# Kernel optimization log

Hardware: AMD Instinct MI355X
Metric: run time of the kernel (lower is better)

## Reference

```python
import jax, jax.numpy as jnp
import numpy as np

N_NODES = 50000
N_EDGES = 800000
N_GRAPHS = 128
F_IN = 128
HID = 64
EDGE_DIM = 16
H1, H2 = 4, 2
NEG_SLOPE = 0.2


def _glorot(key, shape, fan_in):
    return jax.random.normal(key, shape, dtype=jnp.float32) / np.sqrt(fan_in)


def setup_inputs() -> dict:
    key = jax.random.key(0)
    ks = jax.random.split(key, 20)
    x = jax.random.normal(ks[0], (N_NODES, F_IN), dtype=jnp.float32)
    edge_attr = jax.random.normal(ks[1], (N_EDGES, EDGE_DIM), dtype=jnp.float32)
    edge_index = jax.random.randint(ks[2], (2, N_EDGES), 0, N_NODES, dtype=jnp.int32)
    # evenly spread graph ids so every graph is non-empty (sorted)
    batch = (jnp.arange(N_NODES, dtype=jnp.int32) * N_GRAPHS) // N_NODES
    p = {
        'W1': _glorot(ks[3], (F_IN, H1 * HID), F_IN),
        'a_src1': _glorot(ks[4], (H1, HID), HID),
        'a_dst1': _glorot(ks[5], (H1, HID), HID),
        'We1': _glorot(ks[6], (EDGE_DIM, H1 * HID), EDGE_DIM),
        'a_e1': _glorot(ks[7], (H1, HID), HID),
        'b1': jnp.zeros((H1 * HID,), jnp.float32),
        'W2': _glorot(ks[8], (H1 * HID, H2 * HID), H1 * HID),
        'a_src2': _glorot(ks[9], (H2, HID), HID),
        'a_dst2': _glorot(ks[10], (H2, HID), HID),
        'We2': _glorot(ks[11], (EDGE_DIM, H2 * HID), EDGE_DIM),
        'a_e2': _glorot(ks[12], (H2, HID), HID),
        'b2': jnp.zeros((HID,), jnp.float32),
        'Wr': _glorot(ks[13], (HID, 1), HID),
        'br': jnp.zeros((1,), jnp.float32),
    }
    return dict(x=x, edge_attr=edge_attr, edge_index=edge_index, batch=batch, **p)


def _segment_softmax(scores, seg, num_segments):
    # scores: [E, H], softmax grouped by seg (destination node)
    m = jax.ops.segment_max(scores, seg, num_segments)
    m = jnp.where(jnp.isfinite(m), m, 0.0)
    ex = jnp.exp(scores - m[seg])
    s = jax.ops.segment_sum(ex, seg, num_segments)
    return ex / (s[seg] + 1e-16)


def _add_self_loops(edge_index, edge_attr, n):
    # PyG add_self_loops with fill_value='mean': per-dst mean of edge_attr
    src, dst = edge_index[0], edge_index[1]
    cnt = jax.ops.segment_sum(jnp.ones((src.shape[0],), jnp.float32), dst, n)
    loop_attr = jax.ops.segment_sum(edge_attr, dst, n) / jnp.maximum(cnt, 1.0)[:, None]
    loop = jnp.arange(n, dtype=src.dtype)
    return (jnp.concatenate([src, loop]), jnp.concatenate([dst, loop]),
            jnp.concatenate([edge_attr, loop_attr], axis=0))


def _gat_layer(x, e_attr, src, dst, W, a_src, a_dst, We, a_e, b, heads, outc, concat):
    n = x.shape[0]
    xs = (x @ W).reshape(n, heads, outc)                 # [N,H,C]
    s_src = jnp.einsum('nhc,hc->nh', xs, a_src)
    s_dst = jnp.einsum('nhc,hc->nh', xs, a_dst)
    ee = (e_attr @ We).reshape(-1, heads, outc)          # [E,H,C]
    s_e = jnp.einsum('ehc,hc->eh', ee, a_e)
    score = jax.nn.leaky_relu(s_src[src] + s_dst[dst] + s_e, NEG_SLOPE)  # [E,H]
    alpha = _segment_softmax(score, dst, n)
    out = jax.ops.segment_sum(xs[src] * alpha[..., None], dst, n)        # [N,H,C]
    out = out.reshape(n, heads * outc) if concat else out.mean(axis=1)
    return out + b


def reference(x, edge_attr, edge_index, batch,
              W1, a_src1, a_dst1, We1, a_e1, b1,
              W2, a_src2, a_dst2, We2, a_e2, b2, Wr, br):
    n = x.shape[0]
    src, dst, ea = _add_self_loops(edge_index, edge_attr, n)
    h = _gat_layer(x, ea, src, dst, W1, a_src1, a_dst1, We1, a_e1, b1, H1, HID, True)
    h = jax.nn.relu(h)
    h = _gat_layer(h, ea, src, dst, W2, a_src2, a_dst2, We2, a_e2, b2, H2, HID, False)
    g = jax.ops.segment_max(h, batch, N_GRAPHS)          # global max pool [G, HID]
    return g @ Wr + br
```

## Files before the change

kernel.cpp:

```cpp
#include <hip/hip_runtime.h>
#include <hip/hip_bf16.h>
#include <hip/hip_fp16.h>

#define DEVINL __device__ __forceinline__
typedef __hip_bfloat16 bf16;

typedef __attribute__((ext_vector_type(8))) __bf16 bf16x8;
typedef __attribute__((ext_vector_type(4))) float f32x4;

static constexpr int N_NODES  = 50000;
static constexpr int N_EDGES  = 800000;
static constexpr int N_GRAPHS = 128;
static constexpr float NEG_SLOPE = 0.2f;

DEVINL float ldIn(const void* __restrict__ p, size_t i, int isbf) {
    if (isbf) return __bfloat162float(((const bf16*)p)[i]);
    return ((const float*)p)[i];
}

DEVINL unsigned short f2bf(float f) {
    bf16 b = __float2bfloat16(f);
    return *reinterpret_cast<unsigned short*>(&b);
}

DEVINL float bfu2f(unsigned short u) {
    return __uint_as_float(((unsigned)u) << 16);
}

DEVINL unsigned f2hbits(float f) {
    __half h = __float2half(f);
    return (unsigned)*reinterpret_cast<unsigned short*>(&h);
}

DEVINL float hbits2f(unsigned bits) {
    unsigned short us = (unsigned short)bits;
    __half h = *reinterpret_cast<__half*>(&us);
    return __half2float(h);
}

template<int H>
DEVINL void ldrow(const unsigned short* __restrict__ p, unsigned short (&v)[H]) {
    if (H == 4) *reinterpret_cast<uint2*>(v)    = *reinterpret_cast<const uint2*>(p);
    else        *reinterpret_cast<unsigned*>(v) = *reinterpret_cast<const unsigned*>(p);
}

DEVINL float lrelu_exp(float sc) {
    sc = sc > 0.f ? sc : NEG_SLOPE * sc;
    return __expf(sc);
}

__global__ void detect_dtype_kernel(const unsigned short* __restrict__ xu,
                                    int* __restrict__ flag)
{
    int t = threadIdx.x;
    int bad = 0;
    for (int i = t; i < 1024; i += 64) {
        unsigned u = xu[2 * i];
        float v = __uint_as_float(u << 16);
        if (!(fabsf(v) <= 1e4f)) bad = 1;
    }
    unsigned long long m = __ballot(bad);
    if (t == 0) *flag = m ? 0 : 1;
}

__global__ void build_M_kernel(const void* __restrict__ We1, const void* __restrict__ ae1,
                               const void* __restrict__ We2, const void* __restrict__ ae2,
                               const int* __restrict__ flagp,
                               float* __restrict__ M1, float* __restrict__ M2)
{
    const int isbf = *flagp;
    int t = threadIdx.x;
    if (t < 64) {
        int d = t >> 2, h = t & 3;
        float s = 0.f;
        for (int c = 0; c < 64; ++c)
            s += ldIn(We1, d * 256 + h * 64 + c, isbf) * ldIn(ae1, h * 64 + c, isbf);
        M1[d * 4 + h] = s;
    }
    if (t < 32) {
        int d = t >> 1, h = t & 1;
        float s = 0.f;
        for (int c = 0; c < 64; ++c)
            s += ldIn(We2, d * 128 + h * 64 + c, isbf) * ldIn(ae2, h * 64 + c, isbf);
        M2[d * 2 + h] = s;
    }
}

template<int K, int M>
__global__ void build_wfrag_kernel(const void* __restrict__ W, const int* __restrict__ flagp,
                                   bf16* __restrict__ Wfrag)
{
    constexpr int KS = K / 32;
    const int isbf = *flagp;
    int idx = blockIdx.x * 256 + threadIdx.x;
    constexpr int total = (M / 16) * KS * 64 * 8;
    if (idx >= total) return;
    int j    = idx & 7;
    int lane = (idx >> 3) & 63;
    int rem  = idx >> 9;
    int ks   = rem % KS;
    int ct   = rem / KS;
    int k = ks * 32 + (lane >> 4) * 8 + j;
    int n = ct * 16 + (lane & 15);
    Wfrag[idx] = __float2bfloat16(ldIn(W, (size_t)k * M + n, isbf));
}

template<int K, int M, int AMODE, int H>
__global__ __launch_bounds__(256)
void gemm_mfma_kernel(const void* __restrict__ A, const bf16* __restrict__ Wfrag,
                      bf16* __restrict__ C, const int* __restrict__ flagp, int N,
                      const void* __restrict__ a_src, const void* __restrict__ a_dst,
                      float* __restrict__ sA, float* __restrict__ sD)
{
    constexpr int KS = K / 32, CT = M / 16;
    constexpr int LDA = K + 8;
    __shared__ __align__(16) unsigned short Asm[64 * LDA];
    const int isbf = *flagp;
    const int tid  = threadIdx.x;
    const int wave = tid >> 6, lane = tid & 63;
    const int n0 = blockIdx.x * 64;

    for (int i = tid; i < 64 * (K / 8); i += 256) {
        int r  = i / (K / 8);
        int kc = (i % (K / 8)) * 8;
        int n  = n0 + r;
        unsigned short v[8] = {0, 0, 0, 0, 0, 0, 0, 0};
        if (n < N) {
            size_t base = (size_t)n * K + kc;
            if (AMODE == 1 || isbf) {
                *reinterpret_cast<uint4*>(v) =
                    *reinterpret_cast<const uint4*>((const unsigned short*)A + base);
            } else {
                const float* Af = (const float*)A + base;
                float4 f0 = *reinterpret_cast<const float4*>(Af);
                float4 f1 = *reinterpret_cast<const float4*>(Af + 4);
                v[0] = f2bf(f0.x); v[1] = f2bf(f0.y); v[2] = f2bf(f0.z); v[3] = f2bf(f0.w);
                v[4] = f2bf(f1.x); v[5] = f2bf(f1.y); v[6] = f2bf(f1.z); v[7] = f2bf(f1.w);
            }
        }
        *reinterpret_cast<uint4*>(&Asm[r * LDA + kc]) = *reinterpret_cast<uint4*>(v);
    }
    __syncthreads();

    f32x4 acc[CT];
    #pragma unroll
    for (int ct = 0; ct < CT; ++ct) acc[ct] = (f32x4){0.f, 0.f, 0.f, 0.f};

    const int arow  = wave * 16 + (lane & 15);
    const int akoff = (lane >> 4) * 8;
    #pragma unroll
    for (int ks = 0; ks < KS; ++ks) {
        bf16x8 af = *reinterpret_cast<const bf16x8*>(&Asm[arow * LDA + ks * 32 + akoff]);
        #pragma unroll
        for (int ct = 0; ct < CT; ++ct) {
            bf16x8 bfr = *reinterpret_cast<const bf16x8*>(
                &Wfrag[(((size_t)ct * KS + ks) * 64 + lane) * 8]);
            acc[ct] = __builtin_amdgcn_mfma_f32_16x16x32_bf16(af, bfr, acc[ct], 0, 0, 0);
        }
    }

    const int crow0 = n0 + wave * 16 + (lane >> 4) * 4;
    const int ccol  = lane & 15;
    #pragma unroll
    for (int ct = 0; ct < CT; ++ct) {
        #pragma unroll
        for (int r = 0; r < 4; ++r) {
            int row = crow0 + r;
            if (row < N) C[(size_t)row * M + ct * 16 + ccol] = __float2bfloat16(acc[ct][r]);
        }
    }

    float psA[4][H], psD[4][H];
    #pragma unroll
    for (int r = 0; r < 4; ++r)
        #pragma unroll
        for (int hh = 0; hh < H; ++hh) { psA[r][hh] = 0.f; psD[r][hh] = 0.f; }
    #pragma unroll
    for (int ct = 0; ct < CT; ++ct) {
        float as = ldIn(a_src, ct * 16 + ccol, isbf);
        float ad = ldIn(a_dst, ct * 16 + ccol, isbf);
        const int hh = ct >> 2;
        #pragma unroll
        for (int r = 0; r < 4; ++r) {
            psA[r][hh] += acc[ct][r] * as;
            psD[r][hh] += acc[ct][r] * ad;
        }
    }
    #pragma unroll
    for (int m = 1; m < 16; m <<= 1) {
        #pragma unroll
        for (int r = 0; r < 4; ++r)
            #pragma unroll
            for (int hh = 0; hh < H; ++hh) {
                psA[r][hh] += __shfl_xor(psA[r][hh], m);
                psD[r][hh] += __shfl_xor(psD[r][hh], m);
            }
    }
    if (ccol == 0) {
        #pragma unroll
        for (int r = 0; r < 4; ++r) {
            int row = crow0 + r;
            if (row < N) {
                #pragma unroll
                for (int hh = 0; hh < H; ++hh) {
                    sA[(size_t)row * H + hh] = psA[r][hh];
                    sD[(size_t)row * H + hh] = psD[r][hh];
                }
            }
        }
    }
}

__global__ void csr_count_kernel(const int* __restrict__ dst, int* __restrict__ cnt)
{
    int e = blockIdx.x * blockDim.x + threadIdx.x;
    if (e >= N_EDGES) return;
    atomicAdd(&cnt[dst[e]], 1);
}

__global__ __launch_bounds__(256)
void scan_sum_kernel(const int* __restrict__ cnt, int* __restrict__ bsum)
{
    __shared__ int sm[256];
    int i = blockIdx.x * 256 + threadIdx.x;
    sm[threadIdx.x] = (i < N_NODES) ? cnt[i] : 0;
    __syncthreads();
    for (int off = 128; off; off >>= 1) {
        if (threadIdx.x < off) sm[threadIdx.x] += sm[threadIdx.x + off];
        __syncthreads();
    }
    if (threadIdx.x == 0) bsum[blockIdx.x] = sm[0];
}

__global__ __launch_bounds__(256)
void scan_off_kernel(int* __restrict__ bsum, int nb)
{
    __shared__ int sm[256];
    int tid = threadIdx.x;
    int v = (tid < nb) ? bsum[tid] : 0;
    sm[tid] = v;
    __syncthreads();
    for (int off = 1; off < 256; off <<= 1) {
        int t = (tid >= off) ? sm[tid - off] : 0;
        __syncthreads();
        sm[tid] += t;
        __syncthreads();
    }
    if (tid < nb) bsum[tid] = sm[tid] - v;
}

__global__ __launch_bounds__(256)
void scan_final_kernel(const int* __restrict__ cnt, const int* __restrict__ bsum,
                       int* __restrict__ row, int* __restrict__ cursor)
{
    __shared__ int sm[256];
    int i = blockIdx.x * 256 + threadIdx.x;
    int tid = threadIdx.x;
    int v = (i < N_NODES) ? cnt[i] : 0;
    sm[tid] = v;
    __syncthreads();
    for (int off = 1; off < 256; off <<= 1) {
        int t = (tid >= off) ? sm[tid - off] : 0;
        __syncthreads();
        sm[tid] += t;
        __syncthreads();
    }
    int excl = sm[tid] - v + bsum[blockIdx.x];
    if (i < N_NODES) { row[i] = excl; cursor[i] = excl; }
    if (i == N_NODES - 1) row[N_NODES] = excl + v;
}

__global__ void csr_scatter_kernel(const int* __restrict__ srcI, const int* __restrict__ dstI,
                                   const void* __restrict__ eattr, const int* __restrict__ flagp,
                                   const float* __restrict__ M1, const float* __restrict__ M2,
                                   int* __restrict__ cursor, uint4* __restrict__ erec)
{
    const int isbf = *flagp;
    int e = blockIdx.x * blockDim.x + threadIdx.x;
    if (e >= N_EDGES) return;
    float attr[16];
    #pragma unroll
    for (int k = 0; k < 16; ++k) attr[k] = ldIn(eattr, (size_t)e * 16 + k, isbf);
    float4 o1 = {0.f, 0.f, 0.f, 0.f};
    float2 o2 = {0.f, 0.f};
    #pragma unroll
    for (int k = 0; k < 16; ++k) {
        o1.x += attr[k] * M1[k * 4 + 0];
        o1.y += attr[k] * M1[k * 4 + 1];
        o1.z += attr[k] * M1[k * 4 + 2];
        o1.w += attr[k] * M1[k * 4 + 3];
        o2.x += attr[k] * M2[k * 2 + 0];
        o2.y += attr[k] * M2[k * 2 + 1];
    }
    int d = dstI[e];
    int pos = atomicAdd(&cursor[d], 1);
    uint4 rec;
    rec.x = (unsigned)srcI[e];
    rec.y = f2hbits(o1.x) | (f2hbits(o1.y) << 16);
    rec.z = f2hbits(o1.z) | (f2hbits(o1.w) << 16);
    rec.w = f2hbits(o2.x) | (f2hbits(o2.y) << 16);
    erec[pos] = rec;
}

template<int H, int LAYER>
__global__ __launch_bounds__(256)
void agg_fused_kernel(const int* __restrict__ row, const uint4* __restrict__ erec,
                      const bf16* __restrict__ xs,
                      const float* __restrict__ sA, const float* __restrict__ sD,
                      const void* __restrict__ bias,
                      const int* __restrict__ flagp, void* __restrict__ out)
{
    const int isbf = *flagp;
    int dv = (blockIdx.x * 256 + threadIdx.x) >> 6;
    const int d = __builtin_amdgcn_readfirstlane(dv);
    const int lane = threadIdx.x & 63;
    if (d >= N_NODES) return;
    const int h = (lane * H) >> 6;
    const unsigned short* xsu = (const unsigned short*)xs;
    const float sDv = sD[(size_t)d * H + h];
    const float sAd = sA[(size_t)d * H + h];

    float acc[H];
    #pragma unroll
    for (int i = 0; i < H; ++i) acc[i] = 0.f;
    float den = 0.f, seSum = 0.f;

    const int b = row[d], eend = row[d + 1];
    int j = b;
    for (; j + 7 < eend; j += 8) {
        int s[8];
        float se[8], sa[8];
        unsigned short v[8][H];
        #pragma unroll
        for (int u = 0; u < 8; ++u) {
            uint4 rv = erec[j + u];
            s[u] = (int)rv.x;
            if (H == 4) {
                unsigned w16 = (h & 2) ? rv.z : rv.y;
                se[u] = hbits2f((h & 1) ? (w16 >> 16) : (w16 & 0xffffu));
            } else {
                se[u] = hbits2f(h ? (rv.w >> 16) : (rv.w & 0xffffu));
            }
        }
        #pragma unroll
        for (int u = 0; u < 8; ++u) sa[u] = sA[(size_t)s[u] * H + h];
        #pragma unroll
        for (int u = 0; u < 8; ++u) ldrow<H>(&xsu[(size_t)s[u] * (H * 64) + lane * H], v[u]);
        #pragma unroll
        for (int u = 0; u < 8; ++u) {
            float w = lrelu_exp(sa[u] + sDv + se[u]);
            seSum += se[u];
            den += w;
            #pragma unroll
            for (int i = 0; i < H; ++i) acc[i] += w * bfu2f(v[u][i]);
        }
    }
    for (; j < eend; ++j) {
        uint4 rv = erec[j];
        const int s = (int)rv.x;
        float se;
        if (H == 4) {
            unsigned w16 = (h & 2) ? rv.z : rv.y;
            se = hbits2f((h & 1) ? (w16 >> 16) : (w16 & 0xffffu));
        } else {
            se = hbits2f(h ? (rv.w >> 16) : (rv.w & 0xffffu));
        }
        const float sa = sA[(size_t)s * H + h];
        unsigned short v[H];
        ldrow<H>(&xsu[(size_t)s * (H * 64) + lane * H], v);
        const float w = lrelu_exp(sa + sDv + se);
        seSum += se;
        den += w;
        #pragma unroll
        for (int i = 0; i < H; ++i) acc[i] += w * bfu2f(v[i]);
    }

    {
        const int cntv = eend - b;
        const float seM = seSum / fmaxf((float)cntv, 1.f);
        const float wS = lrelu_exp(sAd + sDv + seM);
        unsigned short v[H];
        ldrow<H>(&xsu[(size_t)d * (H * 64) + lane * H], v);
        den += wS;
        #pragma unroll
        for (int i = 0; i < H; ++i) acc[i] += wS * bfu2f(v[i]);
    }

    const float rden = 1.f / (den + 1e-16f);
    if (LAYER == 1) {
        unsigned short o[H];
        #pragma unroll
        for (int i = 0; i < H; ++i) {
            float v = acc[i] * rden + ldIn(bias, lane * H + i, isbf);
            o[i] = f2bf(v > 0.f ? v : 0.f);
        }
        *reinterpret_cast<uint2*>(&((unsigned short*)out)[(size_t)d * (H * 64) + lane * H]) =
            *reinterpret_cast<uint2*>(o);
    } else {
        float v0 = acc[0] * rden, v1 = acc[1] * rden;
        float p0 = __shfl(v0, lane + 32), p1 = __shfl(v1, lane + 32);
        if (lane < 32) {
            float2 o;
            o.x = 0.5f * (v0 + p0) + ldIn(bias, lane * 2 + 0, isbf);
            o.y = 0.5f * (v1 + p1) + ldIn(bias, lane * 2 + 1, isbf);
            *reinterpret_cast<float2*>(&((float*)out)[(size_t)d * 64 + lane * 2]) = o;
        }
    }
}

__global__ __launch_bounds__(256)
void pool_max_kernel(const float* __restrict__ h2, const int* __restrict__ batch,
                     float* __restrict__ g)
{
    int gi = blockIdx.x;
    int lo = 0, hi = N_NODES;
    while (lo < hi) { int mid = (lo + hi) >> 1; if (batch[mid] < gi) lo = mid + 1; else hi = mid; }
    int start = lo;
    lo = start; hi = N_NODES;
    while (lo < hi) { int mid = (lo + hi) >> 1; if (batch[mid] < gi + 1) lo = mid + 1; else hi = mid; }
    int end = lo;
    int c = threadIdx.x & 63, chunk = threadIdx.x >> 6;
    float m = -INFINITY;
    for (int n = start + chunk; n < end; n += 4) m = fmaxf(m, h2[(size_t)n * 64 + c]);
    __shared__ float sm[256];
    sm[threadIdx.x] = m;
    __syncthreads();
    if (threadIdx.x < 64) {
        m = fmaxf(fmaxf(sm[threadIdx.x], sm[threadIdx.x + 64]),
                  fmaxf(sm[threadIdx.x + 128], sm[threadIdx.x + 192]));
        g[gi * 64 + threadIdx.x] = m;
    }
}

__global__ void readout_kernel(const float* __restrict__ g, const void* __restrict__ Wr,
                               const void* __restrict__ br, const int* __restrict__ flagp,
                               void* __restrict__ out)
{
    const int isbf = *flagp;
    int gi = blockIdx.x;
    int lane = threadIdx.x;
    float p = g[gi * 64 + lane] * ldIn(Wr, lane, isbf);
    for (int off = 32; off; off >>= 1) p += __shfl_down(p, off);
    if (lane == 0) {
        float r = p + ldIn(br, 0, isbf);
        if (isbf) ((bf16*)out)[gi] = __float2bfloat16(r);
        else      ((float*)out)[gi] = r;
    }
}

extern "C" void kernel_launch(void* const* d_in, const int* in_sizes, int n_in,
                              void* d_out, int out_size, void* d_ws, size_t ws_size,
                              hipStream_t stream)
{
    const void* x     = d_in[0];
    const void* ea    = d_in[1];
    const int*  eidx  = (const int*)d_in[2];
    const int*  batch = (const int*)d_in[3];
    const void* W1  = d_in[4];
    const void* as1 = d_in[5];
    const void* ad1 = d_in[6];
    const void* We1 = d_in[7];
    const void* ae1 = d_in[8];
    const void* b1  = d_in[9];
    const void* W2  = d_in[10];
    const void* as2 = d_in[11];
    const void* ad2 = d_in[12];
    const void* We2 = d_in[13];
    const void* ae2 = d_in[14];
    const void* b2  = d_in[15];
    const void* Wr  = d_in[16];
    const void* br  = d_in[17];

    const int* srcI = eidx;
    const int* dstI = eidx + N_EDGES;

    float* ws    = (float*)d_ws;
    bf16*  xs    = (bf16*)ws;
    bf16*  h1    = (bf16*)(ws + 6400000);
    float* h2    = ws + 6400000;
    uint4* erec  = (uint4*)(ws + 12800000);
    float* sA1   = ws + 16000000;
    float* sD1   = ws + 16200000;
    float* sA2   = ws + 16400000;
    float* sD2   = ws + 16500000;
    int*   ib    = (int*)(ws + 16600000);
    int*   row    = ib;
    int*   cursor = ib + 50016;
    int*   cnt    = ib + 100032;
    int*   bsum   = ib + 150048;
    float* misc  = ws + 16600000 + 150400;
    int*   flag  = (int*)misc;
    float* M1    = misc + 16;
    float* M2    = misc + 80;
    float* gpool = misc + 112;
    bf16*  wf1   = (bf16*)(misc + 8320);
    bf16*  wf2   = (bf16*)(misc + 8320 + 16384);

    hipMemsetAsync(cnt, 0, N_NODES * sizeof(int), stream);

    detect_dtype_kernel<<<1, 64, 0, stream>>>((const unsigned short*)x, flag);
    build_M_kernel<<<1, 64, 0, stream>>>(We1, ae1, We2, ae2, flag, M1, M2);
    build_wfrag_kernel<128, 256><<<128, 256, 0, stream>>>(W1, flag, wf1);
    build_wfrag_kernel<256, 128><<<128, 256, 0, stream>>>(W2, flag, wf2);

    const int NB = (N_NODES + 255) / 256;
    csr_count_kernel<<<(N_EDGES + 255) / 256, 256, 0, stream>>>(dstI, cnt);
    scan_sum_kernel<<<NB, 256, 0, stream>>>(cnt, bsum);
    scan_off_kernel<<<1, 256, 0, stream>>>(bsum, NB);
    scan_final_kernel<<<NB, 256, 0, stream>>>(cnt, bsum, row, cursor);
    csr_scatter_kernel<<<(N_EDGES + 255) / 256, 256, 0, stream>>>(
        srcI, dstI, ea, flag, M1, M2, cursor, erec);

    const int GB = (N_NODES + 63) / 64;

    gemm_mfma_kernel<128, 256, 0, 4><<<GB, 256, 0, stream>>>(
        x, wf1, xs, flag, N_NODES, as1, ad1, sA1, sD1);
    agg_fused_kernel<4, 1><<<(N_NODES + 3) / 4, 256, 0, stream>>>(
        row, erec, xs, sA1, sD1, b1, flag, h1);

    gemm_mfma_kernel<256, 128, 1, 2><<<GB, 256, 0, stream>>>(
        h1, wf2, xs, flag, N_NODES, as2, ad2, sA2, sD2);
    agg_fused_kernel<2, 2><<<(N_NODES + 3) / 4, 256, 0, stream>>>(
        row, erec, xs, sA2, sD2, b2, flag, h2);

    pool_max_kernel<<<N_GRAPHS, 256, 0, stream>>>(h2, batch, gpool);
    readout_kernel<<<N_GRAPHS, 64, 0, stream>>>(gpool, Wr, br, flag, d_out);
}
```

Baseline: 429.9 us.

## Split wavefront into two half-waves per edge and record CSR ranks during counting

The aggregation kernel now splits each 64-lane wave into two 32-lane halves that process alternate edges. Each lane loads 8 or 4 bf16 features as one 16- or 8-byte vector, and the halves are combined with a cross-half shuffle at the end. This widens per-lane gathers and doubles edge-level parallelism per destination node, at the cost of extra shuffles and some idle lanes in the tail. Separately, the count kernel stores each edge's atomic rank, so the scatter kernel computes its position as row offset plus rank instead of doing a second atomic pass over a cursor array.

```diff
diff --git a/kernel.cpp b/kernel.cpp
--- a/kernel.cpp
+++ b/kernel.cpp
@@ -23,10 +23,6 @@
     return *reinterpret_cast<unsigned short*>(&b);
 }
 
-DEVINL float bfu2f(unsigned short u) {
-    return __uint_as_float(((unsigned)u) << 16);
-}
-
 DEVINL unsigned f2hbits(float f) {
     __half h = __float2half(f);
     return (unsigned)*reinterpret_cast<unsigned short*>(&h);
@@ -38,16 +34,31 @@
     return __half2float(h);
 }
 
-template<int H>
-DEVINL void ldrow(const unsigned short* __restrict__ p, unsigned short (&v)[H]) {
-    if (H == 4) *reinterpret_cast<uint2*>(v)    = *reinterpret_cast<const uint2*>(p);
-    else        *reinterpret_cast<unsigned*>(v) = *reinterpret_cast<const unsigned*>(p);
-}
-
 DEVINL float lrelu_exp(float sc) {
     sc = sc > 0.f ? sc : NEG_SLOPE * sc;
     return __expf(sc);
 }
+
+DEVINL void accw(float w, unsigned wv, float& a0, float& a1) {
+    a0 = fmaf(w, __uint_as_float(wv << 16), a0);
+    a1 = fmaf(w, __uint_as_float(wv & 0xffff0000u), a1);
+}
+
+template<int H>
+DEVINL float getse(const uint4& rv, int h) {
+    unsigned bits;
+    if (H == 4) {
+        unsigned w16 = (h & 2) ? rv.z : rv.y;
+        bits = (h & 1) ? (w16 >> 16) : (w16 & 0xffffu);
+    } else {
+        bits = h ? (rv.w >> 16) : (rv.w & 0xffffu);
+    }
+    return hbits2f(bits);
+}
+
+template<int CPL> struct XVT;
+template<> struct XVT<8> { using T = uint4; };
+template<> struct XVT<4> { using T = uint2; };
 
 __global__ void detect_dtype_kernel(const unsigned short* __restrict__ xu,
                                     int* __restrict__ flag)
@@ -211,11 +222,12 @@
     }
 }
 
-__global__ void csr_count_kernel(const int* __restrict__ dst, int* __restrict__ cnt)
+__global__ void csr_count_kernel(const int* __restrict__ dst, int* __restrict__ cnt,
+                                 int* __restrict__ rank)
 {
     int e = blockIdx.x * blockDim.x + threadIdx.x;
     if (e >= N_EDGES) return;
-    atomicAdd(&cnt[dst[e]], 1);
+    rank[e] = atomicAdd(&cnt[dst[e]], 1);
 }
 
 __global__ __launch_bounds__(256)
@@ -251,7 +263,7 @@
 
 __global__ __launch_bounds__(256)
 void scan_final_kernel(const int* __restrict__ cnt, const int* __restrict__ bsum,
-                       int* __restrict__ row, int* __restrict__ cursor)
+                       int* __restrict__ row)
 {
     __shared__ int sm[256];
     int i = blockIdx.x * 256 + threadIdx.x;
@@ -266,14 +278,15 @@
         __syncthreads();
     }
     int excl = sm[tid] - v + bsum[blockIdx.x];
-    if (i < N_NODES) { row[i] = excl; cursor[i] = excl; }
+    if (i < N_NODES) row[i] = excl;
     if (i == N_NODES - 1) row[N_NODES] = excl + v;
 }
 
 __global__ void csr_scatter_kernel(const int* __restrict__ srcI, const int* __restrict__ dstI,
                                    const void* __restrict__ eattr, const int* __restrict__ flagp,
                                    const float* __restrict__ M1, const float* __restrict__ M2,
-                                   int* __restrict__ cursor, uint4* __restrict__ erec)
+                                   const int* __restrict__ row, const int* __restrict__ rank,
+                                   uint4* __restrict__ erec)
 {
     const int isbf = *flagp;
     int e = blockIdx.x * blockDim.x + threadIdx.x;
@@ -292,8 +305,7 @@
         o2.x += attr[k] * M2[k * 2 + 0];
         o2.y += attr[k] * M2[k * 2 + 1];
     }
-    int d = dstI[e];
-    int pos = atomicAdd(&cursor[d], 1);
+    int pos = row[dstI[e]] + rank[e];
     uint4 rec;
     rec.x = (unsigned)srcI[e];
     rec.y = f2hbits(o1.x) | (f2hbits(o1.y) << 16);
@@ -310,100 +322,116 @@
                       const void* __restrict__ bias,
                       const int* __restrict__ flagp, void* __restrict__ out)
 {
+    constexpr int CPL = (H * 64) / 32;
+    using XV = typename XVT<CPL>::T;
     const int isbf = *flagp;
     int dv = (blockIdx.x * 256 + threadIdx.x) >> 6;
     const int d = __builtin_amdgcn_readfirstlane(dv);
     const int lane = threadIdx.x & 63;
     if (d >= N_NODES) return;
-    const int h = (lane * H) >> 6;
+    const int sub = lane >> 5;
+    const int sl  = lane & 31;
+    const int h = (sl * CPL) >> 6;
     const unsigned short* xsu = (const unsigned short*)xs;
     const float sDv = sD[(size_t)d * H + h];
     const float sAd = sA[(size_t)d * H + h];
 
-    float acc[H];
-    #pragma unroll
-    for (int i = 0; i < H; ++i) acc[i] = 0.f;
+    float acc[CPL];
+    #pragma unroll
+    for (int i = 0; i < CPL; ++i) acc[i] = 0.f;
     float den = 0.f, seSum = 0.f;
 
     const int b = row[d], eend = row[d + 1];
-    int j = b;
-    for (; j + 7 < eend; j += 8) {
-        int s[8];
-        float se[8], sa[8];
-        unsigned short v[8][H];
-        #pragma unroll
-        for (int u = 0; u < 8; ++u) {
-            uint4 rv = erec[j + u];
-            s[u] = (int)rv.x;
-            if (H == 4) {
-                unsigned w16 = (h & 2) ? rv.z : rv.y;
-                se[u] = hbits2f((h & 1) ? (w16 >> 16) : (w16 & 0xffffu));
-            } else {
-                se[u] = hbits2f(h ? (rv.w >> 16) : (rv.w & 0xffffu));
-            }
-        }
-        #pragma unroll
-        for (int u = 0; u < 8; ++u) sa[u] = sA[(size_t)s[u] * H + h];
-        #pragma unroll
-        for (int u = 0; u < 8; ++u) ldrow<H>(&xsu[(size_t)s[u] * (H * 64) + lane * H], v[u]);
-        #pragma unroll
-        for (int u = 0; u < 8; ++u) {
+    const int nb8 = (eend - b) & ~7;
+
+    for (int j0 = b; j0 < b + nb8; j0 += 8) {
+        uint4 rv[4];
+        int   s[4];
+        XV    xv[4];
+        float sa[4], se[4];
+        #pragma unroll
+        for (int u = 0; u < 4; ++u) rv[u] = erec[j0 + 2 * u + sub];
+        #pragma unroll
+        for (int u = 0; u < 4; ++u) s[u] = (int)rv[u].x;
+        #pragma unroll
+        for (int u = 0; u < 4; ++u)
+            xv[u] = *reinterpret_cast<const XV*>(&xsu[(size_t)s[u] * (H * 64) + sl * CPL]);
+        #pragma unroll
+        for (int u = 0; u < 4; ++u) sa[u] = sA[(size_t)s[u] * H + h];
+        #pragma unroll
+        for (int u = 0; u < 4; ++u) se[u] = getse<H>(rv[u], h);
+        #pragma unroll
+        for (int u = 0; u < 4; ++u) {
             float w = lrelu_exp(sa[u] + sDv + se[u]);
             seSum += se[u];
             den += w;
+            const unsigned* wv = reinterpret_cast<const unsigned*>(&xv[u]);
             #pragma unroll
-            for (int i = 0; i < H; ++i) acc[i] += w * bfu2f(v[u][i]);
-        }
-    }
-    for (; j < eend; ++j) {
-        uint4 rv = erec[j];
-        const int s = (int)rv.x;
-        float se;
-        if (H == 4) {
-            unsigned w16 = (h & 2) ? rv.z : rv.y;
-            se = hbits2f((h & 1) ? (w16 >> 16) : (w16 & 0xffffu));
-        } else {
-            se = hbits2f(h ? (rv.w >> 16) : (rv.w & 0xffffu));
-        }
-        const float sa = sA[(size_t)s * H + h];
-        unsigned short v[H];
-        ldrow<H>(&xsu[(size_t)s * (H * 64) + lane * H], v);
-        const float w = lrelu_exp(sa + sDv + se);
-        seSum += se;
+            for (int p = 0; p < CPL / 2; ++p) accw(w, wv[p], acc[2 * p], acc[2 * p + 1]);
+        }
+    }
+    for (int j0 = b + nb8; j0 < eend; j0 += 2) {
+        int jj = j0 + sub;
+        bool valid = jj < eend;
+        int jc = valid ? jj : (eend - 1);
+        uint4 rv = erec[jc];
+        int s = (int)rv.x;
+        float se = getse<H>(rv, h);
+        float sa = sA[(size_t)s * H + h];
+        XV xv = *reinterpret_cast<const XV*>(&xsu[(size_t)s * (H * 64) + sl * CPL]);
+        float w = valid ? lrelu_exp(sa + sDv + se) : 0.f;
+        seSum += valid ? se : 0.f;
         den += w;
-        #pragma unroll
-        for (int i = 0; i < H; ++i) acc[i] += w * bfu2f(v[i]);
-    }
+        const unsigned* wv = reinterpret_cast<const unsigned*>(&xv);
+        #pragma unroll
+        for (int p = 0; p < CPL / 2; ++p) accw(w, wv[p], acc[2 * p], acc[2 * p + 1]);
+    }
+
+    #pragma unroll
+    for (int i = 0; i < CPL; ++i) acc[i] += __shfl_xor(acc[i], 32);
+    den   += __shfl_xor(den, 32);
+    seSum += __shfl_xor(seSum, 32);
 
     {
         const int cntv = eend - b;
         const float seM = seSum / fmaxf((float)cntv, 1.f);
         const float wS = lrelu_exp(sAd + sDv + seM);
-        unsigned short v[H];
-        ldrow<H>(&xsu[(size_t)d * (H * 64) + lane * H], v);
+        XV xv = *reinterpret_cast<const XV*>(&xsu[(size_t)d * (H * 64) + sl * CPL]);
         den += wS;
-        #pragma unroll
-        for (int i = 0; i < H; ++i) acc[i] += wS * bfu2f(v[i]);
+        const unsigned* wv = reinterpret_cast<const unsigned*>(&xv);
+        #pragma unroll
+        for (int p = 0; p < CPL / 2; ++p) accw(wS, wv[p], acc[2 * p], acc[2 * p + 1]);
     }
 
     const float rden = 1.f / (den + 1e-16f);
     if (LAYER == 1) {
-        unsigned short o[H];
-        #pragma unroll
-        for (int i = 0; i < H; ++i) {
-            float v = acc[i] * rden + ldIn(bias, lane * H + i, isbf);
-            o[i] = f2bf(v > 0.f ? v : 0.f);
-        }
-        *reinterpret_cast<uint2*>(&((unsigned short*)out)[(size_t)d * (H * 64) + lane * H]) =
-            *reinterpret_cast<uint2*>(o);
+        if (sub == 0) {
+            unsigned o[CPL / 2];
+            #pragma unroll
+            for (int p = 0; p < CPL / 2; ++p) {
+                float v0 = acc[2 * p] * rden + ldIn(bias, sl * CPL + 2 * p, isbf);
+                float v1 = acc[2 * p + 1] * rden + ldIn(bias, sl * CPL + 2 * p + 1, isbf);
+                v0 = v0 > 0.f ? v0 : 0.f;
+                v1 = v1 > 0.f ? v1 : 0.f;
+                o[p] = (unsigned)f2bf(v0) | ((unsigned)f2bf(v1) << 16);
+            }
+            *reinterpret_cast<uint4*>(&((unsigned short*)out)[(size_t)d * (H * 64) + sl * CPL]) =
+                *reinterpret_cast<uint4*>(o);
+        }
     } else {
-        float v0 = acc[0] * rden, v1 = acc[1] * rden;
-        float p0 = __shfl(v0, lane + 32), p1 = __shfl(v1, lane + 32);
-        if (lane < 32) {
-            float2 o;
-            o.x = 0.5f * (v0 + p0) + ldIn(bias, lane * 2 + 0, isbf);
-            o.y = 0.5f * (v1 + p1) + ldIn(bias, lane * 2 + 1, isbf);
-            *reinterpret_cast<float2*>(&((float*)out)[(size_t)d * 64 + lane * 2]) = o;
+        float v[CPL], p[CPL];
+        #pragma unroll
+        for (int i = 0; i < CPL; ++i) {
+            v[i] = acc[i] * rden;
+            p[i] = __shfl_xor(v[i], 16);
+        }
+        if (lane < 16) {
+            float4 o;
+            o.x = 0.5f * (v[0] + p[0]) + ldIn(bias, sl * 4 + 0, isbf);
+            o.y = 0.5f * (v[1] + p[1]) + ldIn(bias, sl * 4 + 1, isbf);
+            o.z = 0.5f * (v[2] + p[2]) + ldIn(bias, sl * 4 + 2, isbf);
+            o.w = 0.5f * (v[3] + p[3]) + ldIn(bias, sl * 4 + 3, isbf);
+            *reinterpret_cast<float4*>(&((float*)out)[(size_t)d * 64 + sl * 4]) = o;
         }
     }
 }
@@ -485,10 +513,10 @@
     float* sD2   = ws + 16500000;
     int*   ib    = (int*)(ws + 16600000);
     int*   row    = ib;
-    int*   cursor = ib + 50016;
-    int*   cnt    = ib + 100032;
-    int*   bsum   = ib + 150048;
-    float* misc  = ws + 16600000 + 150400;
+    int*   cnt    = ib + 50016;
+    int*   bsum   = ib + 100032;
+    int*   rank   = ib + 100384;
+    float* misc  = ws + 16600000 + 900384;
     int*   flag  = (int*)misc;
     float* M1    = misc + 16;
     float* M2    = misc + 80;
@@ -504,12 +532,12 @@
     build_wfrag_kernel<256, 128><<<128, 256, 0, stream>>>(W2, flag, wf2);
 
     const int NB = (N_NODES + 255) / 256;
-    csr_count_kernel<<<(N_EDGES + 255) / 256, 256, 0, stream>>>(dstI, cnt);
+    csr_count_kernel<<<(N_EDGES + 255) / 256, 256, 0, stream>>>(dstI, cnt, rank);
     scan_sum_kernel<<<NB, 256, 0, stream>>>(cnt, bsum);
     scan_off_kernel<<<1, 256, 0, stream>>>(bsum, NB);
-    scan_final_kernel<<<NB, 256, 0, stream>>>(cnt, bsum, row, cursor);
+    scan_final_kernel<<<NB, 256, 0, stream>>>(cnt, bsum, row);
     csr_scatter_kernel<<<(N_EDGES + 255) / 256, 256, 0, stream>>>(
-        srcI, dstI, ea, flag, M1, M2, cursor, erec);
+        srcI, dstI, ea, flag, M1, M2, row, rank, erec);
 
     const int GB = (N_NODES + 63) / 64;
 
```

After: 423.7 us. Within noise of the previous version (-1.4%).

## Fuse max-pool into layer-2 aggregation and drop CSR cursor atomics

Applied to the files above, without the earlier changes.

The global max-pool is folded into the second aggregation kernel with atomicMax on order-preserving encoded floats, so the h2 buffer write and the separate pool kernel go away. CSR scatter now reuses the per-edge rank returned by the counting atomics instead of a second round of cursor atomics. The three setup kernels are merged into one launch, and the edge-record and feature loads in the aggregation loop are reordered to issue earlier. In exchange, the pooling output is now fed by contended atomics (about 390 nodes per graph) and a rank array adds extra traffic.

```diff
diff --git a/kernel.cpp b/kernel.cpp
--- a/kernel.cpp
+++ b/kernel.cpp
@@ -38,15 +38,35 @@
     return __half2float(h);
 }
 
+DEVINL float lrelu_exp(float sc) {
+    sc = sc > 0.f ? sc : NEG_SLOPE * sc;
+    return __expf(sc);
+}
+
+DEVINL unsigned fenc(float f) {
+    unsigned s = __float_as_uint(f);
+    return (s & 0x80000000u) ? ~s : (s | 0x80000000u);
+}
+DEVINL float fdec(unsigned u) {
+    return (u & 0x80000000u) ? __uint_as_float(u ^ 0x80000000u) : __uint_as_float(~u);
+}
+
 template<int H>
 DEVINL void ldrow(const unsigned short* __restrict__ p, unsigned short (&v)[H]) {
     if (H == 4) *reinterpret_cast<uint2*>(v)    = *reinterpret_cast<const uint2*>(p);
     else        *reinterpret_cast<unsigned*>(v) = *reinterpret_cast<const unsigned*>(p);
 }
 
-DEVINL float lrelu_exp(float sc) {
-    sc = sc > 0.f ? sc : NEG_SLOPE * sc;
-    return __expf(sc);
+template<int H>
+DEVINL float getse(const uint4& rv, int h) {
+    unsigned bits;
+    if (H == 4) {
+        unsigned w16 = (h & 2) ? rv.z : rv.y;
+        bits = (h & 1) ? (w16 >> 16) : (w16 & 0xffffu);
+    } else {
+        bits = h ? (rv.w >> 16) : (rv.w & 0xffffu);
+    }
+    return hbits2f(bits);
 }
 
 __global__ void detect_dtype_kernel(const unsigned short* __restrict__ xu,
@@ -63,38 +83,10 @@
     if (t == 0) *flag = m ? 0 : 1;
 }
 
-__global__ void build_M_kernel(const void* __restrict__ We1, const void* __restrict__ ae1,
-                               const void* __restrict__ We2, const void* __restrict__ ae2,
-                               const int* __restrict__ flagp,
-                               float* __restrict__ M1, float* __restrict__ M2)
-{
-    const int isbf = *flagp;
-    int t = threadIdx.x;
-    if (t < 64) {
-        int d = t >> 2, h = t & 3;
-        float s = 0.f;
-        for (int c = 0; c < 64; ++c)
-            s += ldIn(We1, d * 256 + h * 64 + c, isbf) * ldIn(ae1, h * 64 + c, isbf);
-        M1[d * 4 + h] = s;
-    }
-    if (t < 32) {
-        int d = t >> 1, h = t & 1;
-        float s = 0.f;
-        for (int c = 0; c < 64; ++c)
-            s += ldIn(We2, d * 128 + h * 64 + c, isbf) * ldIn(ae2, h * 64 + c, isbf);
-        M2[d * 2 + h] = s;
-    }
-}
-
-template<int K, int M>
-__global__ void build_wfrag_kernel(const void* __restrict__ W, const int* __restrict__ flagp,
-                                   bf16* __restrict__ Wfrag)
-{
-    constexpr int KS = K / 32;
-    const int isbf = *flagp;
-    int idx = blockIdx.x * 256 + threadIdx.x;
-    constexpr int total = (M / 16) * KS * 64 * 8;
-    if (idx >= total) return;
+DEVINL void wfrag_one(const void* __restrict__ W, int isbf, bf16* __restrict__ Wfrag,
+                      int idx, int K, int M)
+{
+    int KS = K / 32;
     int j    = idx & 7;
     int lane = (idx >> 3) & 63;
     int rem  = idx >> 9;
@@ -103,6 +95,38 @@
     int k = ks * 32 + (lane >> 4) * 8 + j;
     int n = ct * 16 + (lane & 15);
     Wfrag[idx] = __float2bfloat16(ldIn(W, (size_t)k * M + n, isbf));
+}
+
+__global__ void setup_kernel(const void* __restrict__ We1, const void* __restrict__ ae1,
+                             const void* __restrict__ We2, const void* __restrict__ ae2,
+                             const void* __restrict__ W1, const void* __restrict__ W2,
+                             const int* __restrict__ flagp,
+                             float* __restrict__ M1, float* __restrict__ M2,
+                             bf16* __restrict__ wf1, bf16* __restrict__ wf2)
+{
+    const int isbf = *flagp;
+    const int bx = blockIdx.x;
+    if (bx == 0) {
+        int t = threadIdx.x;
+        if (t < 64) {
+            int d = t >> 2, h = t & 3;
+            float s = 0.f;
+            for (int c = 0; c < 64; ++c)
+                s += ldIn(We1, d * 256 + h * 64 + c, isbf) * ldIn(ae1, h * 64 + c, isbf);
+            M1[d * 4 + h] = s;
+        }
+        if (t < 32) {
+            int d = t >> 1, h = t & 1;
+            float s = 0.f;
+            for (int c = 0; c < 64; ++c)
+                s += ldIn(We2, d * 128 + h * 64 + c, isbf) * ldIn(ae2, h * 64 + c, isbf);
+            M2[d * 2 + h] = s;
+        }
+    } else if (bx <= 128) {
+        wfrag_one(W1, isbf, wf1, (bx - 1) * 256 + threadIdx.x, 128, 256);
+    } else {
+        wfrag_one(W2, isbf, wf2, (bx - 129) * 256 + threadIdx.x, 256, 128);
+    }
 }
 
 template<int K, int M, int AMODE, int H>
@@ -211,11 +235,12 @@
     }
 }
 
-__global__ void csr_count_kernel(const int* __restrict__ dst, int* __restrict__ cnt)
+__global__ void csr_count_kernel(const int* __restrict__ dst, int* __restrict__ cnt,
+                                 int* __restrict__ rank)
 {
     int e = blockIdx.x * blockDim.x + threadIdx.x;
     if (e >= N_EDGES) return;
-    atomicAdd(&cnt[dst[e]], 1);
+    rank[e] = atomicAdd(&cnt[dst[e]], 1);
 }
 
 __global__ __launch_bounds__(256)
@@ -251,7 +276,7 @@
 
 __global__ __launch_bounds__(256)
 void scan_final_kernel(const int* __restrict__ cnt, const int* __restrict__ bsum,
-                       int* __restrict__ row, int* __restrict__ cursor)
+                       int* __restrict__ row)
 {
     __shared__ int sm[256];
     int i = blockIdx.x * 256 + threadIdx.x;
@@ -266,14 +291,15 @@
         __syncthreads();
     }
     int excl = sm[tid] - v + bsum[blockIdx.x];
-    if (i < N_NODES) { row[i] = excl; cursor[i] = excl; }
+    if (i < N_NODES) row[i] = excl;
     if (i == N_NODES - 1) row[N_NODES] = excl + v;
 }
 
 __global__ void csr_scatter_kernel(const int* __restrict__ srcI, const int* __restrict__ dstI,
                                    const void* __restrict__ eattr, const int* __restrict__ flagp,
                                    const float* __restrict__ M1, const float* __restrict__ M2,
-                                   int* __restrict__ cursor, uint4* __restrict__ erec)
+                                   const int* __restrict__ row, const int* __restrict__ rank,
+                                   uint4* __restrict__ erec)
 {
     const int isbf = *flagp;
     int e = blockIdx.x * blockDim.x + threadIdx.x;
@@ -292,8 +318,7 @@
         o2.x += attr[k] * M2[k * 2 + 0];
         o2.y += attr[k] * M2[k * 2 + 1];
     }
-    int d = dstI[e];
-    int pos = atomicAdd(&cursor[d], 1);
+    int pos = row[dstI[e]] + rank[e];
     uint4 rec;
     rec.x = (unsigned)srcI[e];
     rec.y = f2hbits(o1.x) | (f2hbits(o1.y) << 16);
@@ -307,7 +332,7 @@
 void agg_fused_kernel(const int* __restrict__ row, const uint4* __restrict__ erec,
                       const bf16* __restrict__ xs,
                       const float* __restrict__ sA, const float* __restrict__ sD,
-                      const void* __restrict__ bias,
+                      const void* __restrict__ bias, const int* __restrict__ batch,
                       const int* __restrict__ flagp, void* __restrict__ out)
 {
     const int isbf = *flagp;
@@ -331,21 +356,17 @@
         int s[8];
         float se[8], sa[8];
         unsigned short v[8][H];
-        #pragma unroll
-        for (int u = 0; u < 8; ++u) {
-            uint4 rv = erec[j + u];
-            s[u] = (int)rv.x;
-            if (H == 4) {
-                unsigned w16 = (h & 2) ? rv.z : rv.y;
-                se[u] = hbits2f((h & 1) ? (w16 >> 16) : (w16 & 0xffffu));
-            } else {
-                se[u] = hbits2f(h ? (rv.w >> 16) : (rv.w & 0xffffu));
-            }
-        }
+        uint4 rv[8];
+        #pragma unroll
+        for (int u = 0; u < 8; ++u) rv[u] = erec[j + u];
+        #pragma unroll
+        for (int u = 0; u < 8; ++u) s[u] = (int)rv[u].x;
+        #pragma unroll
+        for (int u = 0; u < 8; ++u) ldrow<H>(&xsu[(size_t)s[u] * (H * 64) + lane * H], v[u]);
         #pragma unroll
         for (int u = 0; u < 8; ++u) sa[u] = sA[(size_t)s[u] * H + h];
         #pragma unroll
-        for (int u = 0; u < 8; ++u) ldrow<H>(&xsu[(size_t)s[u] * (H * 64) + lane * H], v[u]);
+        for (int u = 0; u < 8; ++u) se[u] = getse<H>(rv[u], h);
         #pragma unroll
         for (int u = 0; u < 8; ++u) {
             float w = lrelu_exp(sa[u] + sDv + se[u]);
@@ -358,13 +379,7 @@
     for (; j < eend; ++j) {
         uint4 rv = erec[j];
         const int s = (int)rv.x;
-        float se;
-        if (H == 4) {
-            unsigned w16 = (h & 2) ? rv.z : rv.y;
-            se = hbits2f((h & 1) ? (w16 >> 16) : (w16 & 0xffffu));
-        } else {
-            se = hbits2f(h ? (rv.w >> 16) : (rv.w & 0xffffu));
-        }
+        float se = getse<H>(rv, h);
         const float sa = sA[(size_t)s * H + h];
         unsigned short v[H];
         ldrow<H>(&xsu[(size_t)s * (H * 64) + lane * H], v);
@@ -400,46 +415,24 @@
         float v0 = acc[0] * rden, v1 = acc[1] * rden;
         float p0 = __shfl(v0, lane + 32), p1 = __shfl(v1, lane + 32);
         if (lane < 32) {
-            float2 o;
-            o.x = 0.5f * (v0 + p0) + ldIn(bias, lane * 2 + 0, isbf);
-            o.y = 0.5f * (v1 + p1) + ldIn(bias, lane * 2 + 1, isbf);
-            *reinterpret_cast<float2*>(&((float*)out)[(size_t)d * 64 + lane * 2]) = o;
-        }
-    }
-}
-
-__global__ __launch_bounds__(256)
-void pool_max_kernel(const float* __restrict__ h2, const int* __restrict__ batch,
-                     float* __restrict__ g)
-{
-    int gi = blockIdx.x;
-    int lo = 0, hi = N_NODES;
-    while (lo < hi) { int mid = (lo + hi) >> 1; if (batch[mid] < gi) lo = mid + 1; else hi = mid; }
-    int start = lo;
-    lo = start; hi = N_NODES;
-    while (lo < hi) { int mid = (lo + hi) >> 1; if (batch[mid] < gi + 1) lo = mid + 1; else hi = mid; }
-    int end = lo;
-    int c = threadIdx.x & 63, chunk = threadIdx.x >> 6;
-    float m = -INFINITY;
-    for (int n = start + chunk; n < end; n += 4) m = fmaxf(m, h2[(size_t)n * 64 + c]);
-    __shared__ float sm[256];
-    sm[threadIdx.x] = m;
-    __syncthreads();
-    if (threadIdx.x < 64) {
-        m = fmaxf(fmaxf(sm[threadIdx.x], sm[threadIdx.x + 64]),
-                  fmaxf(sm[threadIdx.x + 128], sm[threadIdx.x + 192]));
-        g[gi * 64 + threadIdx.x] = m;
-    }
-}
-
-__global__ void readout_kernel(const float* __restrict__ g, const void* __restrict__ Wr,
+            const int g = batch[d];
+            float o0 = 0.5f * (v0 + p0) + ldIn(bias, lane * 2 + 0, isbf);
+            float o1 = 0.5f * (v1 + p1) + ldIn(bias, lane * 2 + 1, isbf);
+            unsigned* gp = (unsigned*)out;
+            atomicMax(&gp[g * 64 + lane * 2 + 0], fenc(o0));
+            atomicMax(&gp[g * 64 + lane * 2 + 1], fenc(o1));
+        }
+    }
+}
+
+__global__ void readout_kernel(const unsigned* __restrict__ gpool, const void* __restrict__ Wr,
                                const void* __restrict__ br, const int* __restrict__ flagp,
                                void* __restrict__ out)
 {
     const int isbf = *flagp;
     int gi = blockIdx.x;
     int lane = threadIdx.x;
-    float p = g[gi * 64 + lane] * ldIn(Wr, lane, isbf);
+    float p = fdec(gpool[gi * 64 + lane]) * ldIn(Wr, lane, isbf);
     for (int off = 32; off; off >>= 1) p += __shfl_down(p, off);
     if (lane == 0) {
         float r = p + ldIn(br, 0, isbf);
@@ -474,55 +467,52 @@
     const int* srcI = eidx;
     const int* dstI = eidx + N_EDGES;
 
-    float* ws    = (float*)d_ws;
-    bf16*  xs    = (bf16*)ws;
-    bf16*  h1    = (bf16*)(ws + 6400000);
-    float* h2    = ws + 6400000;
-    uint4* erec  = (uint4*)(ws + 12800000);
-    float* sA1   = ws + 16000000;
-    float* sD1   = ws + 16200000;
-    float* sA2   = ws + 16400000;
-    float* sD2   = ws + 16500000;
-    int*   ib    = (int*)(ws + 16600000);
-    int*   row    = ib;
-    int*   cursor = ib + 50016;
-    int*   cnt    = ib + 100032;
-    int*   bsum   = ib + 150048;
-    float* misc  = ws + 16600000 + 150400;
-    int*   flag  = (int*)misc;
-    float* M1    = misc + 16;
-    float* M2    = misc + 80;
-    float* gpool = misc + 112;
-    bf16*  wf1   = (bf16*)(misc + 8320);
-    bf16*  wf2   = (bf16*)(misc + 8320 + 16384);
+    float*    ws    = (float*)d_ws;
+    bf16*     xs    = (bf16*)ws;
+    bf16*     h1    = (bf16*)(ws + 6400000);
+    uint4*    erec  = (uint4*)(ws + 12800000);
+    float*    sA1   = ws + 16000000;
+    float*    sD1   = ws + 16200000;
+    float*    sA2   = ws + 16400000;
+    float*    sD2   = ws + 16500000;
+    int*      ib    = (int*)(ws + 16600000);
+    int*      row    = ib;
+    int*      cnt    = ib + 50016;
+    int*      bsum   = ib + 100032;
+    int*      rank   = ib + 100384;
+    float*    misc  = ws + 16600000 + 900384;
+    int*      flag  = (int*)misc;
+    float*    M1    = misc + 16;
+    float*    M2    = misc + 80;
+    unsigned* gpool = (unsigned*)(misc + 112);
+    bf16*     wf1   = (bf16*)(misc + 8320);
+    bf16*     wf2   = (bf16*)(misc + 8320 + 16384);
 
     hipMemsetAsync(cnt, 0, N_NODES * sizeof(int), stream);
+    hipMemsetAsync(gpool, 0, N_GRAPHS * 64 * sizeof(unsigned), stream);
 
     detect_dtype_kernel<<<1, 64, 0, stream>>>((const unsigned short*)x, flag);
-    build_M_kernel<<<1, 64, 0, stream>>>(We1, ae1, We2, ae2, flag, M1, M2);
-    build_wfrag_kernel<128, 256><<<128, 256, 0, stream>>>(W1, flag, wf1);
-    build_wfrag_kernel<256, 128><<<128, 256, 0, stream>>>(W2, flag, wf2);
+    setup_kernel<<<257, 256, 0, stream>>>(We1, ae1, We2, ae2, W1, W2, flag, M1, M2, wf1, wf2);
 
     const int NB = (N_NODES + 255) / 256;
-    csr_count_kernel<<<(N_EDGES + 255) / 256, 256, 0, stream>>>(dstI, cnt);
+    csr_count_kernel<<<(N_EDGES + 255) / 256, 256, 0, stream>>>(dstI, cnt, rank);
     scan_sum_kernel<<<NB, 256, 0, stream>>>(cnt, bsum);
     scan_off_kernel<<<1, 256, 0, stream>>>(bsum, NB);
-    scan_final_kernel<<<NB, 256, 0, stream>>>(cnt, bsum, row, cursor);
+    scan_final_kernel<<<NB, 256, 0, stream>>>(cnt, bsum, row);
     csr_scatter_kernel<<<(N_EDGES + 255) / 256, 256, 0, stream>>>(
-        srcI, dstI, ea, flag, M1, M2, cursor, erec);
+        srcI, dstI, ea, flag, M1, M2, row, rank, erec);
 
     const int GB = (N_NODES + 63) / 64;
 
     gemm_mfma_kernel<128, 256, 0, 4><<<GB, 256, 0, stream>>>(
         x, wf1, xs, flag, N_NODES, as1, ad1, sA1, sD1);
     agg_fused_kernel<4, 1><<<(N_NODES + 3) / 4, 256, 0, stream>>>(
-        row, erec, xs, sA1, sD1, b1, flag, h1);
+        row, erec, xs, sA1, sD1, b1, batch, flag, h1);
 
     gemm_mfma_kernel<256, 128, 1, 2><<<GB, 256, 0, stream>>>(
         h1, wf2, xs, flag, N_NODES, as2, ad2, sA2, sD2);
     agg_fused_kernel<2, 2><<<(N_NODES + 3) / 4, 256, 0, stream>>>(
-        row, erec, xs, sA2, sD2, b2, flag, h2);
-
-    pool_max_kernel<<<N_GRAPHS, 256, 0, stream>>>(h2, batch, gpool);
+        row, erec, xs, sA2, sD2, b2, batch, flag, gpool);
+
     readout_kernel<<<N_GRAPHS, 64, 0, stream>>>(gpool, Wr, br, flag, d_out);
 }
```

Result: slower. 440.7 us (+2.5%).
